# Optimization experiments

Measured on AMD Instinct MI355X. Metric: run time of the kernel, lower is better.

Reference implementation:

```python
import jax, jax.numpy as jnp
import numpy as np

N_NODES = 50000
N_EDGES = 800000
IN_DIM = 768
HID = 128
NUM_CLASSES = 6


def setup_inputs() -> dict:
    key = jax.random.key(0)
    ks = jax.random.split(key, 8)
    x = jax.random.normal(ks[0], (N_NODES, IN_DIM), dtype=jnp.float32)
    edge_index = jax.random.randint(ks[1], (2, N_EDGES), 0, N_NODES, dtype=jnp.int64)
    W1 = jax.random.normal(ks[2], (IN_DIM, HID), dtype=jnp.float32) / np.sqrt(IN_DIM)
    b1 = jnp.zeros((HID,), dtype=jnp.float32)
    W2 = jax.random.normal(ks[3], (HID, HID), dtype=jnp.float32) / np.sqrt(HID)
    b2 = jnp.zeros((HID,), dtype=jnp.float32)
    Wi = jax.random.normal(ks[4], (HID, NUM_CLASSES), dtype=jnp.float32) / np.sqrt(HID)
    bi = jnp.zeros((NUM_CLASSES,), dtype=jnp.float32)
    Wl = jax.random.normal(ks[5], (HID, NUM_CLASSES), dtype=jnp.float32) / np.sqrt(HID)
    bl = jnp.zeros((NUM_CLASSES,), dtype=jnp.float32)
    return {"x": x, "edge_index": edge_index, "W1": W1, "b1": b1,
            "W2": W2, "b2": b2, "Wi": Wi, "bi": bi, "Wl": Wl, "bl": bl}


def gcn_conv(x, src, dst, norm, W, b, num_nodes):
    # PyG GCNConv: h = x W; out[i] = sum_{j->i} norm_ji * h[j] + b
    h = x @ W                                   # [N, out_dim]
    msg = h[src] * norm[:, None]                # [E+N, out_dim] gather
    out = jax.ops.segment_sum(msg, dst, num_segments=num_nodes)  # scatter-add
    return out + b


def reference(x, edge_index, W1, b1, W2, b2, Wi, bi, Wl, bl):
    num_nodes = x.shape[0]
    ei = jnp.clip(edge_index, 0, num_nodes - 1)
    # add self-loops (PyG GCNConv default)
    loop = jnp.arange(num_nodes, dtype=ei.dtype)
    src = jnp.concatenate([ei[0], loop])
    dst = jnp.concatenate([ei[1], loop])
    # symmetric degree normalization deg^-1/2 (deg >= 1 due to self-loops)
    deg = jax.ops.segment_sum(jnp.ones_like(dst, dtype=x.dtype), dst,
                              num_segments=num_nodes)
    dinv = jax.lax.rsqrt(jnp.maximum(deg, 1.0))
    norm = dinv[src] * dinv[dst]                # [E+N]

    h = jax.nn.relu(gcn_conv(x, src, dst, norm, W1, b1, num_nodes))
    # dropout is identity at inference (eval mode)
    h = jax.nn.relu(gcn_conv(h, src, dst, norm, W2, b2, num_nodes))
    impact = jax.nn.log_softmax(h @ Wi + bi, axis=1)
    likelihood = jax.nn.log_softmax(h @ Wl + bl, axis=1)
    return (impact, likelihood)
```

## Files before the change

### kernel.cpp

```cpp
#include <hip/hip_runtime.h>
#include <hip/hip_bf16.h>

#define NN 50000
#define NE 800000
#define KD 768
#define HIDD 128
#define NC 6
#define PADW 64
#define OVCAP 262144

typedef __attribute__((ext_vector_type(8))) short bf16x8;
typedef __attribute__((ext_vector_type(4))) float f32x4;

__device__ __forceinline__ ushort f2bf(float f) {
    union { float f; unsigned u; } v; v.f = f;
    unsigned u = v.u + 0x7FFF + ((v.u >> 16) & 1);
    return (ushort)(u >> 16);
}
__device__ __forceinline__ float bf2f(ushort h) {
    union { unsigned u; float f; } v; v.u = ((unsigned)h) << 16;
    return v.f;
}
__device__ __forceinline__ void gll16(const void* g, void* l) {
    __builtin_amdgcn_global_load_lds((const __attribute__((address_space(1))) void*)g,
                                     (__attribute__((address_space(3))) void*)l, 16, 0, 0);
}


template <int KTOT>
__device__ __forceinline__ void pack_granule(const float* __restrict__ W,
                                             ushort* __restrict__ WTp, int gi) {
    const int KS = KTOT / 64;
    int ci = gi / (KS * 64);
    int rem = gi % (KS * 64);
    int ks = rem >> 6;
    int lane = rem & 63;
    int lr = lane >> 3;
    int lg = (lane & 7) ^ lr;
    int c = ci * 8 + lr;
    ushort tmp[8];
#pragma unroll
    for (int j = 0; j < 8; ++j)
        tmp[j] = f2bf(W[(size_t)(ks * 64 + lg * 8 + j) * HIDD + c]);
    *(bf16x8*)&WTp[(size_t)gi * 8] = *(bf16x8*)tmp;
}


__global__ void pack_fill_kernel(const int* __restrict__ ei, int* __restrict__ cnt,
                                 int* __restrict__ pad_col, int* __restrict__ ov_cnt,
                                 int2* __restrict__ ov,
                                 const float* __restrict__ W1, const float* __restrict__ W2,
                                 ushort* __restrict__ WT1p, ushort* __restrict__ WT2p) {
    const int PB = 56;
    const int G1 = 16 * (KD / 64) * 64;
    const int G2 = 16 * (HIDD / 64) * 64;
    int b = blockIdx.x;
    if (b < PB) {
        int gi = b * 256 + threadIdx.x;
        if (gi < G1) pack_granule<KD>(W1, WT1p, gi);
        else if (gi < G1 + G2) pack_granule<HIDD>(W2, WT2p, gi - G1);
        return;
    }
    int e = (b - PB) * 256 + threadIdx.x;
    int sidx = ei[e];
    int d = ei[NE + e];
    sidx = min(max(sidx, 0), NN - 1);
    d = min(max(d, 0), NN - 1);
    int pos = atomicAdd(&cnt[d], 1);
    if (pos < PADW) {
        pad_col[(size_t)d * PADW + pos] = sidx;
    } else {
        int op = atomicAdd(ov_cnt, 1);
        if (op < OVCAP) ov[op] = make_int2(d, sidx);
    }
}


__global__ __launch_bounds__(256) void gemm1_dinv_kernel(
    const float* __restrict__ A, const ushort* __restrict__ WTp,
    const int* __restrict__ cnt, float* __restrict__ dinv,
    ushort* __restrict__ out, int M) {
    const int GB = (NN + 63) / 64;
    __shared__ ushort As[64 * 64];
    __shared__ ushort Bs[128 * 64];
    if (blockIdx.x >= GB) {
        int i = (blockIdx.x - GB) * 256 + threadIdx.x;
        if (i < NN) dinv[i] = rsqrtf((float)(cnt[i] + 1));
        return;
    }
    const int KS = KD / 64;
    int t = threadIdx.x;
    int lane = t & 63;
    int wid = t >> 6;
    int wr = wid >> 1, wc = wid & 1;
    int row0 = blockIdx.x * 64;
    f32x4 acc[2][4] = {};

    for (int ks = 0; ks < KS; ++ks) {
        int k0 = ks * 64;
#pragma unroll
        for (int it = 0; it < 4; ++it) {
            int r = (t >> 4) + it * 16;
            int k4 = t & 15;
            int gr = min(row0 + r, M - 1);
            float4 v = *(const float4*)&A[(size_t)gr * KD + k0 + k4 * 4];
            ushort4 w;
            w.x = f2bf(v.x); w.y = f2bf(v.y); w.z = f2bf(v.z); w.w = f2bf(v.w);
            int g = k4 >> 1, half = k4 & 1;
            *(ushort4*)&As[r * 64 + ((g ^ (r & 7)) * 8) + half * 4] = w;
        }
#pragma unroll
        for (int it = 0; it < 4; ++it) {
            int ci = wid * 4 + it;
            gll16(&WTp[(size_t)((ci * KS + ks) * 64 + lane) * 8], &Bs[ci * 512]);
        }
        __syncthreads();
#pragma unroll
        for (int h = 0; h < 2; ++h) {
            int q = h * 4 + (lane >> 4);
            bf16x8 a[2];
#pragma unroll
            for (int m = 0; m < 2; ++m) {
                int r = wr * 32 + m * 16 + (lane & 15);
                a[m] = *(const bf16x8*)&As[r * 64 + (q ^ (r & 7)) * 8];
            }
#pragma unroll
            for (int n = 0; n < 4; ++n) {
                int c = wc * 64 + n * 16 + (lane & 15);
                bf16x8 b = *(const bf16x8*)&Bs[c * 64 + (q ^ (c & 7)) * 8];
#pragma unroll
                for (int m = 0; m < 2; ++m)
                    acc[m][n] = __builtin_amdgcn_mfma_f32_16x16x32_bf16(a[m], b, acc[m][n], 0, 0, 0);
            }
        }
        __syncthreads();
    }
#pragma unroll
    for (int m = 0; m < 2; ++m) {
#pragma unroll
        for (int reg = 0; reg < 4; ++reg) {
            int row = row0 + wr * 32 + m * 16 + (lane >> 4) * 4 + reg;
            if (row < M) {
#pragma unroll
                for (int n = 0; n < 4; ++n) {
                    int colg = wc * 64 + n * 16 + (lane & 15);
                    out[(size_t)row * 128 + colg] = f2bf(acc[m][n][reg]);
                }
            }
        }
    }
}


__global__ __launch_bounds__(256) void mfma_gemm2(const ushort* __restrict__ A,
                                                  const ushort* __restrict__ WTp,
                                                  const float* __restrict__ dinv,
                                                  ushort* __restrict__ out, int M) {
    const int KS = HIDD / 64;
    __shared__ ushort As[64 * 64];
    __shared__ ushort Bs[128 * 64];
    int t = threadIdx.x;
    int lane = t & 63;
    int wid = t >> 6;
    int wr = wid >> 1, wc = wid & 1;
    int row0 = blockIdx.x * 64;
    f32x4 acc[2][4] = {};

    int lr = lane >> 3;
    int lg = (lane & 7) ^ lr;

    for (int ks = 0; ks < KS; ++ks) {
        int k0 = ks * 64;
#pragma unroll
        for (int it = 0; it < 2; ++it) {
            int ci2 = wid * 2 + it;
            int r = ci2 * 8 + lr;
            int gr = min(row0 + r, M - 1);
            gll16(&A[(size_t)gr * HIDD + k0 + lg * 8], &As[ci2 * 512]);
        }
#pragma unroll
        for (int it = 0; it < 4; ++it) {
            int ci = wid * 4 + it;
            gll16(&WTp[(size_t)((ci * KS + ks) * 64 + lane) * 8], &Bs[ci * 512]);
        }
        __syncthreads();
#pragma unroll
        for (int h = 0; h < 2; ++h) {
            int q = h * 4 + (lane >> 4);
            bf16x8 a[2];
#pragma unroll
            for (int m = 0; m < 2; ++m) {
                int r = wr * 32 + m * 16 + (lane & 15);
                a[m] = *(const bf16x8*)&As[r * 64 + (q ^ (r & 7)) * 8];
            }
#pragma unroll
            for (int n = 0; n < 4; ++n) {
                int c = wc * 64 + n * 16 + (lane & 15);
                bf16x8 b = *(const bf16x8*)&Bs[c * 64 + (q ^ (c & 7)) * 8];
#pragma unroll
                for (int m = 0; m < 2; ++m)
                    acc[m][n] = __builtin_amdgcn_mfma_f32_16x16x32_bf16(a[m], b, acc[m][n], 0, 0, 0);
            }
        }
        __syncthreads();
    }
#pragma unroll
    for (int m = 0; m < 2; ++m) {
#pragma unroll
        for (int reg = 0; reg < 4; ++reg) {
            int row = row0 + wr * 32 + m * 16 + (lane >> 4) * 4 + reg;
            if (row < M) {
                float d = dinv[row];
#pragma unroll
                for (int n = 0; n < 4; ++n) {
                    int colg = wc * 64 + n * 16 + (lane & 15);
                    out[(size_t)row * 128 + colg] = f2bf(acc[m][n][reg] * d);
                }
            }
        }
    }
}


__device__ __forceinline__ void acc_edge(float& ax, float& ay, unsigned w) {
    ax += bf2f((ushort)(w & 0xffff));
    ay += bf2f((ushort)(w >> 16));
}

template <int U>
__device__ __forceinline__ int gather_tier_d(const ushort* __restrict__ hs,
                                             const int* __restrict__ cols,
                                             const float* __restrict__ dinv,
                                             int e, int e1, int l, float& ax, float& ay) {
    for (; e + U <= e1; e += U) {
        int j[U];
#pragma unroll
        for (int u = 0; u < U; ++u) j[u] = cols[e + u];
        unsigned w[U];
        float dj[U];
#pragma unroll
        for (int u = 0; u < U; ++u) {
            w[u] = *(const unsigned*)&hs[(size_t)j[u] * 128 + 2 * l];
            dj[u] = dinv[j[u]];
        }
#pragma unroll
        for (int u = 0; u < U; ++u) {
            ax = fmaf(dj[u], bf2f((ushort)(w[u] & 0xffff)), ax);
            ay = fmaf(dj[u], bf2f((ushort)(w[u] >> 16)), ay);
        }
    }
    return e;
}

template <int U>
__device__ __forceinline__ int gather_tier(const ushort* __restrict__ hs,
                                           const int* __restrict__ cols,
                                           int e, int e1, int l, float& ax, float& ay) {
    for (; e + U <= e1; e += U) {
        unsigned w[U];
#pragma unroll
        for (int u = 0; u < U; ++u)
            w[u] = *(const unsigned*)&hs[(size_t)cols[e + u] * 128 + 2 * l];
#pragma unroll
        for (int u = 0; u < U; ++u) acc_edge(ax, ay, w[u]);
    }
    return e;
}


__global__ void agg1_kernel(const ushort* __restrict__ hs, const int* __restrict__ cnt,
                            const int* __restrict__ pad_col, const float* __restrict__ dinv,
                            const float* __restrict__ bias,
                            const int* __restrict__ ov_cnt, const int2* __restrict__ ov,
                            ushort* __restrict__ out) {
    int wv = threadIdx.x >> 6;
    int l = threadIdx.x & 63;
    int i = blockIdx.x * 4 + wv;
    float d = dinv[i];
    unsigned v0 = *(const unsigned*)&hs[(size_t)i * 128 + 2 * l];
    float ax = d * bf2f((ushort)(v0 & 0xffff));
    float ay = d * bf2f((ushort)(v0 >> 16));
    int deg = cnt[i];
    int n = min(deg, PADW);
    const int* cols = pad_col + (size_t)i * PADW;
    int e = 0;
    e = gather_tier_d<16>(hs, cols, dinv, e, n, l, ax, ay);
    e = gather_tier_d<8>(hs, cols, dinv, e, n, l, ax, ay);
    e = gather_tier_d<4>(hs, cols, dinv, e, n, l, ax, ay);
    for (; e < n; ++e) {
        int j = cols[e];
        unsigned w = *(const unsigned*)&hs[(size_t)j * 128 + 2 * l];
        float dj = dinv[j];
        ax = fmaf(dj, bf2f((ushort)(w & 0xffff)), ax);
        ay = fmaf(dj, bf2f((ushort)(w >> 16)), ay);
    }
    if (deg > PADW) {
        int oc = min(*ov_cnt, OVCAP);
        for (int k = 0; k < oc; ++k) {
            int2 pr = ov[k];
            if (pr.x == i) {
                unsigned w = *(const unsigned*)&hs[(size_t)pr.y * 128 + 2 * l];
                float dj = dinv[pr.y];
                ax = fmaf(dj, bf2f((ushort)(w & 0xffff)), ax);
                ay = fmaf(dj, bf2f((ushort)(w >> 16)), ay);
            }
        }
    }
    float ox = fmaxf(fmaf(ax, d, bias[2 * l]), 0.f);
    float oy = fmaxf(fmaf(ay, d, bias[2 * l + 1]), 0.f);
    unsigned o = (unsigned)f2bf(ox) | ((unsigned)f2bf(oy) << 16);
    *(unsigned*)&out[(size_t)i * 128 + 2 * l] = o;
}


__global__ void agg2_heads_kernel(const ushort* __restrict__ hs, const int* __restrict__ cnt,
                                  const int* __restrict__ pad_col, const float* __restrict__ dinv,
                                  const float* __restrict__ bias,
                                  const int* __restrict__ ov_cnt, const int2* __restrict__ ov,
                                  const float* __restrict__ Wi, const float* __restrict__ bi,
                                  const float* __restrict__ Wl, const float* __restrict__ bl,
                                  float* __restrict__ out) {
    int wv = threadIdx.x >> 6;
    int l = threadIdx.x & 63;
    int i = blockIdx.x * 4 + wv;
    unsigned v0 = *(const unsigned*)&hs[(size_t)i * 128 + 2 * l];
    float ax = bf2f((ushort)(v0 & 0xffff));
    float ay = bf2f((ushort)(v0 >> 16));
    int deg = cnt[i];
    int n = min(deg, PADW);
    const int* cols = pad_col + (size_t)i * PADW;
    int e = 0;
    e = gather_tier<16>(hs, cols, e, n, l, ax, ay);
    e = gather_tier<8>(hs, cols, e, n, l, ax, ay);
    e = gather_tier<4>(hs, cols, e, n, l, ax, ay);
    for (; e < n; ++e)
        acc_edge(ax, ay, *(const unsigned*)&hs[(size_t)cols[e] * 128 + 2 * l]);
    if (deg > PADW) {
        int oc = min(*ov_cnt, OVCAP);
        for (int k = 0; k < oc; ++k) {
            int2 pr = ov[k];
            if (pr.x == i)
                acc_edge(ax, ay, *(const unsigned*)&hs[(size_t)pr.y * 128 + 2 * l]);
        }
    }
    float d = dinv[i];
    float ox = fmaxf(fmaf(ax, d, bias[2 * l]), 0.f);
    float oy = fmaxf(fmaf(ay, d, bias[2 * l + 1]), 0.f);

    float4 u0 = *(const float4*)&Wi[l * 12];
    float4 u1 = *(const float4*)&Wi[l * 12 + 4];
    float4 u2 = *(const float4*)&Wi[l * 12 + 8];
    float pi[6];
    pi[0] = ox * u0.x + oy * u1.z;
    pi[1] = ox * u0.y + oy * u1.w;
    pi[2] = ox * u0.z + oy * u2.x;
    pi[3] = ox * u0.w + oy * u2.y;
    pi[4] = ox * u1.x + oy * u2.z;
    pi[5] = ox * u1.y + oy * u2.w;
    u0 = *(const float4*)&Wl[l * 12];
    u1 = *(const float4*)&Wl[l * 12 + 4];
    u2 = *(const float4*)&Wl[l * 12 + 8];
    float pl[6];
    pl[0] = ox * u0.x + oy * u1.z;
    pl[1] = ox * u0.y + oy * u1.w;
    pl[2] = ox * u0.z + oy * u2.x;
    pl[3] = ox * u0.w + oy * u2.y;
    pl[4] = ox * u1.x + oy * u2.z;
    pl[5] = ox * u1.y + oy * u2.w;
#pragma unroll
    for (int off = 1; off < 64; off <<= 1) {
#pragma unroll
        for (int c = 0; c < 6; ++c) {
            pi[c] += __shfl_xor(pi[c], off);
            pl[c] += __shfl_xor(pl[c], off);
        }
    }
#pragma unroll
    for (int c = 0; c < 6; ++c) {
        pi[c] += bi[c];
        pl[c] += bl[c];
    }
    float mi = fmaxf(fmaxf(fmaxf(pi[0], pi[1]), fmaxf(pi[2], pi[3])), fmaxf(pi[4], pi[5]));
    float ml = fmaxf(fmaxf(fmaxf(pl[0], pl[1]), fmaxf(pl[2], pl[3])), fmaxf(pl[4], pl[5]));
    float si = 0.f, sl = 0.f;
#pragma unroll
    for (int c = 0; c < 6; ++c) {
        si += expf(pi[c] - mi);
        sl += expf(pl[c] - ml);
    }
    float lsi = mi + logf(si), lsl = ml + logf(sl);
#pragma unroll
    for (int c = 0; c < 6; ++c) {
        if (l == c)     out[(size_t)i * NC + c] = pi[c] - lsi;
        if (l == 6 + c) out[(size_t)NN * NC + (size_t)i * NC + c] = pl[c] - lsl;
    }
}

extern "C" void kernel_launch(void* const* d_in, const int* in_sizes, int n_in,
                              void* d_out, int out_size, void* d_ws, size_t ws_size,
                              hipStream_t stream) {
    const float* x  = (const float*)d_in[0];
    const int*   ei = (const int*)d_in[1];
    const float* W1 = (const float*)d_in[2];
    const float* b1 = (const float*)d_in[3];
    const float* W2 = (const float*)d_in[4];
    const float* b2 = (const float*)d_in[5];
    const float* Wi = (const float*)d_in[6];
    const float* bi = (const float*)d_in[7];
    const float* Wl = (const float*)d_in[8];
    const float* bl = (const float*)d_in[9];
    float* out = (float*)d_out;

    uint8_t* p = (uint8_t*)d_ws;
    auto alloc = [&](size_t bytes) {
        void* r = (void*)p;
        p += (bytes + 255) / 256 * 256;
        return r;
    };
    int* cnt      = (int*)alloc((NN + 64) * sizeof(int));
    int* pad_col  = (int*)alloc((size_t)NN * PADW * sizeof(int));
    int2* ov      = (int2*)alloc((size_t)OVCAP * sizeof(int2));
    float* dinv   = (float*)alloc(NN * sizeof(float));
    ushort* WT1p  = (ushort*)alloc((size_t)KD * HIDD * sizeof(ushort));
    ushort* WT2p  = (ushort*)alloc((size_t)HIDD * HIDD * sizeof(ushort));
    ushort* bufA  = (ushort*)alloc((size_t)NN * HIDD * sizeof(ushort));
    ushort* bufB  = (ushort*)alloc((size_t)NN * HIDD * sizeof(ushort));
    int* ov_cnt = cnt + NN;

    const int FB = NE / 256;
    const int PB = 56;
    const int GB = (NN + 63) / 64;
    const int DB = (NN + 255) / 256;

    hipMemsetAsync(cnt, 0, (NN + 64) * sizeof(int), stream);
    pack_fill_kernel<<<PB + FB, 256, 0, stream>>>(ei, cnt, pad_col, ov_cnt, ov,
                                                  W1, W2, WT1p, WT2p);
    gemm1_dinv_kernel<<<GB + DB, 256, 0, stream>>>(x, WT1p, cnt, dinv, bufA, NN);
    agg1_kernel<<<NN / 4, 256, 0, stream>>>(bufA, cnt, pad_col, dinv, b1, ov_cnt, ov, bufB);
    mfma_gemm2<<<GB, 256, 0, stream>>>(bufB, WT2p, dinv, bufA, NN);
    agg2_heads_kernel<<<NN / 4, 256, 0, stream>>>(bufA, cnt, pad_col, dinv, b2, ov_cnt, ov,
                                                  Wi, bi, Wl, bl, out);
}
```

Before: 192.4 us.

## Overlap edge bucketing with GEMM1 and compute degree norm inline

The memset becomes a zero-fill inside the weight-packing kernel, and the edge bucketing (atomic fill of padded adjacency) moves into the GEMM1 launch as extra blocks so it can run alongside the dense matmul. The separate dinv array and its compute pass are removed; each consumer recomputes rsqrt(cnt+1) on the fly. This cuts one launch and one memset and lets the scattered atomics overlap with compute. In exchange, the aggregation gathers now read cnt and recompute rsqrt per neighbor edge.

Measured after the change: 174.6 us. 9.2% less time.

```diff
diff --git a/kernel.cpp b/kernel.cpp
--- a/kernel.cpp
+++ b/kernel.cpp
@@ -24,6 +24,9 @@
 __device__ __forceinline__ void gll16(const void* g, void* l) {
     __builtin_amdgcn_global_load_lds((const __attribute__((address_space(1))) void*)g,
                                      (__attribute__((address_space(3))) void*)l, 16, 0, 0);
+}
+__device__ __forceinline__ float dinv_of(int c) {
+    return rsqrtf((float)(c + 1));
 }
 
 
@@ -46,9 +49,7 @@
 }
 
 
-__global__ void pack_fill_kernel(const int* __restrict__ ei, int* __restrict__ cnt,
-                                 int* __restrict__ pad_col, int* __restrict__ ov_cnt,
-                                 int2* __restrict__ ov,
+__global__ void pack_zero_kernel(int* __restrict__ cnt,
                                  const float* __restrict__ W1, const float* __restrict__ W2,
                                  ushort* __restrict__ WT1p, ushort* __restrict__ WT2p) {
     const int PB = 56;
@@ -59,33 +60,34 @@
         int gi = b * 256 + threadIdx.x;
         if (gi < G1) pack_granule<KD>(W1, WT1p, gi);
         else if (gi < G1 + G2) pack_granule<HIDD>(W2, WT2p, gi - G1);
-        return;
-    }
-    int e = (b - PB) * 256 + threadIdx.x;
-    int sidx = ei[e];
-    int d = ei[NE + e];
-    sidx = min(max(sidx, 0), NN - 1);
-    d = min(max(d, 0), NN - 1);
-    int pos = atomicAdd(&cnt[d], 1);
-    if (pos < PADW) {
-        pad_col[(size_t)d * PADW + pos] = sidx;
     } else {
-        int op = atomicAdd(ov_cnt, 1);
-        if (op < OVCAP) ov[op] = make_int2(d, sidx);
-    }
-}
-
-
-__global__ __launch_bounds__(256) void gemm1_dinv_kernel(
+        int i = (b - PB) * 256 + threadIdx.x;
+        if (i < NN + 64) cnt[i] = 0;
+    }
+}
+
+
+__global__ __launch_bounds__(256) void gemm1_fill_kernel(
     const float* __restrict__ A, const ushort* __restrict__ WTp,
-    const int* __restrict__ cnt, float* __restrict__ dinv,
-    ushort* __restrict__ out, int M) {
+    ushort* __restrict__ out, int M,
+    const int* __restrict__ ei, int* __restrict__ cnt,
+    int* __restrict__ pad_col, int* __restrict__ ov_cnt, int2* __restrict__ ov) {
     const int GB = (NN + 63) / 64;
     __shared__ ushort As[64 * 64];
     __shared__ ushort Bs[128 * 64];
     if (blockIdx.x >= GB) {
-        int i = (blockIdx.x - GB) * 256 + threadIdx.x;
-        if (i < NN) dinv[i] = rsqrtf((float)(cnt[i] + 1));
+        int e = (blockIdx.x - GB) * 256 + threadIdx.x;
+        int sidx = ei[e];
+        int d = ei[NE + e];
+        sidx = min(max(sidx, 0), NN - 1);
+        d = min(max(d, 0), NN - 1);
+        int pos = atomicAdd(&cnt[d], 1);
+        if (pos < PADW) {
+            pad_col[(size_t)d * PADW + pos] = sidx;
+        } else {
+            int op = atomicAdd(ov_cnt, 1);
+            if (op < OVCAP) ov[op] = make_int2(d, sidx);
+        }
         return;
     }
     const int KS = KD / 64;
@@ -154,7 +156,7 @@
 
 __global__ __launch_bounds__(256) void mfma_gemm2(const ushort* __restrict__ A,
                                                   const ushort* __restrict__ WTp,
-                                                  const float* __restrict__ dinv,
+                                                  const int* __restrict__ cnt,
                                                   ushort* __restrict__ out, int M) {
     const int KS = HIDD / 64;
     __shared__ ushort As[64 * 64];
@@ -210,7 +212,7 @@
         for (int reg = 0; reg < 4; ++reg) {
             int row = row0 + wr * 32 + m * 16 + (lane >> 4) * 4 + reg;
             if (row < M) {
-                float d = dinv[row];
+                float d = dinv_of(cnt[row]);
 #pragma unroll
                 for (int n = 0; n < 4; ++n) {
                     int colg = wc * 64 + n * 16 + (lane & 15);
@@ -230,7 +232,7 @@
 template <int U>
 __device__ __forceinline__ int gather_tier_d(const ushort* __restrict__ hs,
                                              const int* __restrict__ cols,
-                                             const float* __restrict__ dinv,
+                                             const int* __restrict__ cnt,
                                              int e, int e1, int l, float& ax, float& ay) {
     for (; e + U <= e1; e += U) {
         int j[U];
@@ -241,7 +243,7 @@
 #pragma unroll
         for (int u = 0; u < U; ++u) {
             w[u] = *(const unsigned*)&hs[(size_t)j[u] * 128 + 2 * l];
-            dj[u] = dinv[j[u]];
+            dj[u] = dinv_of(cnt[j[u]]);
         }
 #pragma unroll
         for (int u = 0; u < U; ++u) {
@@ -269,28 +271,28 @@
 
 
 __global__ void agg1_kernel(const ushort* __restrict__ hs, const int* __restrict__ cnt,
-                            const int* __restrict__ pad_col, const float* __restrict__ dinv,
+                            const int* __restrict__ pad_col,
                             const float* __restrict__ bias,
                             const int* __restrict__ ov_cnt, const int2* __restrict__ ov,
                             ushort* __restrict__ out) {
     int wv = threadIdx.x >> 6;
     int l = threadIdx.x & 63;
     int i = blockIdx.x * 4 + wv;
-    float d = dinv[i];
+    int deg = cnt[i];
+    float d = dinv_of(deg);
     unsigned v0 = *(const unsigned*)&hs[(size_t)i * 128 + 2 * l];
     float ax = d * bf2f((ushort)(v0 & 0xffff));
     float ay = d * bf2f((ushort)(v0 >> 16));
-    int deg = cnt[i];
     int n = min(deg, PADW);
     const int* cols = pad_col + (size_t)i * PADW;
     int e = 0;
-    e = gather_tier_d<16>(hs, cols, dinv, e, n, l, ax, ay);
-    e = gather_tier_d<8>(hs, cols, dinv, e, n, l, ax, ay);
-    e = gather_tier_d<4>(hs, cols, dinv, e, n, l, ax, ay);
+    e = gather_tier_d<16>(hs, cols, cnt, e, n, l, ax, ay);
+    e = gather_tier_d<8>(hs, cols, cnt, e, n, l, ax, ay);
+    e = gather_tier_d<4>(hs, cols, cnt, e, n, l, ax, ay);
     for (; e < n; ++e) {
         int j = cols[e];
         unsigned w = *(const unsigned*)&hs[(size_t)j * 128 + 2 * l];
-        float dj = dinv[j];
+        float dj = dinv_of(cnt[j]);
         ax = fmaf(dj, bf2f((ushort)(w & 0xffff)), ax);
         ay = fmaf(dj, bf2f((ushort)(w >> 16)), ay);
     }
@@ -300,7 +302,7 @@
             int2 pr = ov[k];
             if (pr.x == i) {
                 unsigned w = *(const unsigned*)&hs[(size_t)pr.y * 128 + 2 * l];
-                float dj = dinv[pr.y];
+                float dj = dinv_of(cnt[pr.y]);
                 ax = fmaf(dj, bf2f((ushort)(w & 0xffff)), ax);
                 ay = fmaf(dj, bf2f((ushort)(w >> 16)), ay);
             }
@@ -314,7 +316,7 @@
 
 
 __global__ void agg2_heads_kernel(const ushort* __restrict__ hs, const int* __restrict__ cnt,
-                                  const int* __restrict__ pad_col, const float* __restrict__ dinv,
+                                  const int* __restrict__ pad_col,
                                   const float* __restrict__ bias,
                                   const int* __restrict__ ov_cnt, const int2* __restrict__ ov,
                                   const float* __restrict__ Wi, const float* __restrict__ bi,
@@ -343,7 +345,7 @@
                 acc_edge(ax, ay, *(const unsigned*)&hs[(size_t)pr.y * 128 + 2 * l]);
         }
     }
-    float d = dinv[i];
+    float d = dinv_of(deg);
     float ox = fmaxf(fmaf(ax, d, bias[2 * l]), 0.f);
     float oy = fmaxf(fmaf(ay, d, bias[2 * l + 1]), 0.f);
 
@@ -420,7 +422,6 @@
     int* cnt      = (int*)alloc((NN + 64) * sizeof(int));
     int* pad_col  = (int*)alloc((size_t)NN * PADW * sizeof(int));
     int2* ov      = (int2*)alloc((size_t)OVCAP * sizeof(int2));
-    float* dinv   = (float*)alloc(NN * sizeof(float));
     ushort* WT1p  = (ushort*)alloc((size_t)KD * HIDD * sizeof(ushort));
     ushort* WT2p  = (ushort*)alloc((size_t)HIDD * HIDD * sizeof(ushort));
     ushort* bufA  = (ushort*)alloc((size_t)NN * HIDD * sizeof(ushort));
@@ -429,15 +430,14 @@
 
     const int FB = NE / 256;
     const int PB = 56;
+    const int ZB = (NN + 64 + 255) / 256;
     const int GB = (NN + 63) / 64;
-    const int DB = (NN + 255) / 256;
-
-    hipMemsetAsync(cnt, 0, (NN + 64) * sizeof(int), stream);
-    pack_fill_kernel<<<PB + FB, 256, 0, stream>>>(ei, cnt, pad_col, ov_cnt, ov,
-                                                  W1, W2, WT1p, WT2p);
-    gemm1_dinv_kernel<<<GB + DB, 256, 0, stream>>>(x, WT1p, cnt, dinv, bufA, NN);
-    agg1_kernel<<<NN / 4, 256, 0, stream>>>(bufA, cnt, pad_col, dinv, b1, ov_cnt, ov, bufB);
-    mfma_gemm2<<<GB, 256, 0, stream>>>(bufB, WT2p, dinv, bufA, NN);
-    agg2_heads_kernel<<<NN / 4, 256, 0, stream>>>(bufA, cnt, pad_col, dinv, b2, ov_cnt, ov,
+
+    pack_zero_kernel<<<PB + ZB, 256, 0, stream>>>(cnt, W1, W2, WT1p, WT2p);
+    gemm1_fill_kernel<<<GB + FB, 256, 0, stream>>>(x, WT1p, bufA, NN,
+                                                   ei, cnt, pad_col, ov_cnt, ov);
+    agg1_kernel<<<NN / 4, 256, 0, stream>>>(bufA, cnt, pad_col, b1, ov_cnt, ov, bufB);
+    mfma_gemm2<<<GB, 256, 0, stream>>>(bufB, WT2p, cnt, bufA, NN);
+    agg2_heads_kernel<<<NN / 4, 256, 0, stream>>>(bufA, cnt, pad_col, b2, ov_cnt, ov,
                                                   Wi, bi, Wl, bl, out);
 }
```
